# Optimization experiments

Hardware: AMD Instinct MI355X
Metric: run time of the kernel (lower is better)

Reference implementation:

```python
import jax, jax.numpy as jnp
import numpy as np

N = 20000   # num_nodes
D = 128     # node_dim
H = 128     # hidden_dim (also per-head channels, PyG out_channels is per-head)
EV = 64     # event_dim
NH = 4      # heads
E = 250000  # num edges
NT = 8      # num_event_types
K = 4       # active event types


def setup_inputs() -> dict:
    key = jax.random.key(0)
    ks = jax.random.split(key, 24)
    def w(i, shape, s=0.05):
        return jax.random.normal(ks[i], shape, dtype=jnp.float32) * s
    z = lambda shape: jnp.zeros(shape, jnp.float32)
    o = lambda shape: jnp.ones(shape, jnp.float32)
    return {
        "node_ids": jnp.arange(N, dtype=jnp.int32),
        "event_type_ids": jax.random.randint(ks[0], (K,), 0, NT, dtype=jnp.int32),
        "src": jax.random.randint(ks[1], (E,), 0, N, dtype=jnp.int32),
        "dst": jax.random.randint(ks[2], (E,), 0, N, dtype=jnp.int32),
        "event_features": jax.random.normal(ks[3], (EV,), dtype=jnp.float32),
        "event_intensity": jax.random.uniform(ks[4], (K,), dtype=jnp.float32),
        "node_emb_table": w(5, (N, D), 1.0),
        "event_type_table": w(6, (NT, H), 0.5),
        "ev_w1": w(7, (EV, H)), "ev_b1": z((H,)), "ev_g1": o((H,)), "ev_bt1": z((H,)),
        "ev_w2": w(8, (H, H)), "ev_b2": z((H,)), "ev_g2": o((H,)), "ev_bt2": z((H,)),
        "wq": w(9, (D + H, NH * H)), "bq": z((NH * H,)),
        "wk": w(10, (D + H, NH * H)), "bk": z((NH * H,)),
        "wv": w(11, (D + H, NH * H)), "bv": z((NH * H,)),
        "wskip": w(12, (D + H, H)), "bskip": z((H,)),
        "g0_w": w(13, (H, NH * H)), "g0_as": w(14, (NH, H), 0.1), "g0_ad": w(15, (NH, H), 0.1), "g0_b": z((H,)),
        "g1_w": w(16, (H, NH * H)), "g1_as": w(17, (NH, H), 0.1), "g1_ad": w(18, (NH, H), 0.1), "g1_b": z((H,)),
        "wih": w(19, (H, 4 * H)), "whh": w(20, (H, 4 * H)), "bih": z((4 * H,)), "bhh": z((4 * H,)),
    }


def layer_norm(x, g, b, eps=1e-5):
    mu = jnp.mean(x, axis=-1, keepdims=True)
    var = jnp.mean(jnp.square(x - mu), axis=-1, keepdims=True)
    return (x - mu) * jax.lax.rsqrt(var + eps) * g + b


def segment_softmax(logits, seg, n):
    # logits: [E, NH]; softmax over edges sharing the same destination seg id
    m = jax.ops.segment_max(logits, seg, num_segments=n)
    m = jnp.where(jnp.isfinite(m), m, 0.0)  # guard empty segments
    e = jnp.exp(logits - m[seg])
    s = jax.ops.segment_sum(e, seg, num_segments=n)
    return e / (s[seg] + 1e-16)


def _forward(node_ids, event_type_ids, src, dst,
             event_features, event_intensity, node_emb_table, event_type_table,
             ev_w1, ev_b1, ev_g1, ev_bt1, ev_w2, ev_b2, ev_g2, ev_bt2,
             wq, bq, wk, bk, wv, bv, wskip, bskip,
             g0_w, g0_as, g0_ad, g0_b, g1_w, g1_as, g1_ad, g1_b,
             wih, whh, bih, bhh):
    node_emb = node_emb_table[node_ids]                                      # [N, D]
    # event encoder MLP (dropout off / eval mode)
    e = jax.nn.relu(layer_norm(event_features @ ev_w1 + ev_b1, ev_g1, ev_bt1))
    e = jax.nn.relu(layer_norm(e @ ev_w2 + ev_b2, ev_g2, ev_bt2))            # [H]
    # intensity-weighted mean of active event-type embeddings
    e = e + jnp.mean(event_type_table[event_type_ids] * event_intensity[:, None], axis=0)
    x = jnp.concatenate([node_emb, jnp.broadcast_to(e, (N, H))], axis=1)     # [N, D+H]

    # --- TransformerConv (heads=NH, concat=False -> head mean, root_weight skip) ---
    q = (x @ wq + bq).reshape(N, NH, H)
    k = (x @ wk + bk).reshape(N, NH, H)
    v = (x @ wv + bv).reshape(N, NH, H)
    alpha = jnp.sum(q[dst] * k[src], axis=-1) / jnp.sqrt(jnp.float32(H))     # [E, NH]
    alpha = segment_softmax(alpha, dst, N)
    agg = jax.ops.segment_sum(v[src] * alpha[..., None], dst, num_segments=N)  # [N, NH, H]
    x = agg.mean(axis=1) + x @ wskip + bskip                                 # [N, H]

    sl = jnp.arange(N, dtype=src.dtype)
    src2 = jnp.concatenate([src, sl])
    dst2 = jnp.concatenate([dst, sl])
    for w_, asrc, adst, b_ in ((g0_w, g0_as, g0_ad, g0_b), (g1_w, g1_as, g1_ad, g1_b)):
        xh = (x @ w_).reshape(N, NH, H)
        a_s = jnp.sum(xh * asrc, axis=-1)                                    # [N, NH]
        a_d = jnp.sum(xh * adst, axis=-1)
        ee = jax.nn.leaky_relu(a_s[src2] + a_d[dst2], 0.2)                   # [E+N, NH]
        a = segment_softmax(ee, dst2, N)
        out = jax.ops.segment_sum(xh[src2] * a[..., None], dst2, num_segments=N)
        x = jax.nn.relu(out.mean(axis=1) + b_)                               # [N, H]

    # --- batched LSTMCell, zero initial (h, c); torch gate order i, f, g, o ---
    h0 = jnp.zeros((N, H), x.dtype)
    c0 = jnp.zeros((N, H), x.dtype)
    gates = x @ wih + bih + h0 @ whh + bhh                                   # [N, 4H]
    gi, gf, gg, go = jnp.split(gates, 4, axis=-1)
    c = jax.nn.sigmoid(gf) * c0 + jax.nn.sigmoid(gi) * jnp.tanh(gg)
    h = jax.nn.sigmoid(go) * jnp.tanh(c)
    return h, c


def reference(node_ids, event_type_ids, src, dst,
              event_features, event_intensity, node_emb_table, event_type_table,
              ev_w1, ev_b1, ev_g1, ev_bt1, ev_w2, ev_b2, ev_g2, ev_bt2,
              wq, bq, wk, bk, wv, bv, wskip, bskip,
              g0_w, g0_as, g0_ad, g0_b, g1_w, g1_as, g1_ad, g1_b,
              wih, whh, bih, bhh):
    return _forward(node_ids, event_type_ids, src, dst,
                    event_features, event_intensity, node_emb_table, event_type_table,
                    ev_w1, ev_b1, ev_g1, ev_bt1, ev_w2, ev_b2, ev_g2, ev_bt2,
                    wq, bq, wk, bk, wv, bv, wskip, bskip,
                    g0_w, g0_as, g0_ad, g0_b, g1_w, g1_as, g1_ad, g1_b,
                    wih, whh, bih, bhh)
```

## Files before the change

### kernel.cpp

```cpp
#include <hip/hip_runtime.h>
#include <math.h>

#define D_DIM 128
#define H_DIM 128
#define SQRT_H_INV 0.08838834764831845f
#define BCOL_QKV 0
#define BCOL_G0 1664
#define BCOL_G1 2176
#define BCOL_W  2688
#define BCOL_TOT 3072

typedef unsigned short u16;
typedef unsigned short ushort8v __attribute__((ext_vector_type(8)));
typedef __bf16 bf16x8 __attribute__((ext_vector_type(8)));
typedef float f32x4 __attribute__((ext_vector_type(4)));

__device__ __forceinline__ float grp16_sum(float v) {
  v += __shfl_xor(v, 1);
  v += __shfl_xor(v, 2);
  v += __shfl_xor(v, 4);
  v += __shfl_xor(v, 8);
  return v;
}

__device__ __forceinline__ void split_bf16(float x, u16& h, u16& l) {
  __bf16 hb = (__bf16)x;
  float rm = x - (float)hb;
  __bf16 lb = (__bf16)rm;
  h = __builtin_bit_cast(u16, hb);
  l = __builtin_bit_cast(u16, lb);
}

__global__ __launch_bounds__(128) void k_event(
    const float* __restrict__ ef, int EV,
    const float* __restrict__ w1, const float* __restrict__ b1,
    const float* __restrict__ g1, const float* __restrict__ bt1,
    const float* __restrict__ w2, const float* __restrict__ b2,
    const float* __restrict__ g2, const float* __restrict__ bt2,
    const float* __restrict__ ett, const int* __restrict__ etid,
    const float* __restrict__ inten, int K,
    float* __restrict__ e_out)
{
  __shared__ float sh[H_DIM];
  __shared__ float red[H_DIM];
  const int t = threadIdx.x;

  float acc = b1[t];
  for (int i = 0; i < EV; ++i) acc += ef[i] * w1[i * H_DIM + t];

  red[t] = acc; __syncthreads();
  for (int s = 64; s > 0; s >>= 1) { if (t < s) red[t] += red[t + s]; __syncthreads(); }
  float mu = red[0] / H_DIM; __syncthreads();
  float d = acc - mu;
  red[t] = d * d; __syncthreads();
  for (int s = 64; s > 0; s >>= 1) { if (t < s) red[t] += red[t + s]; __syncthreads(); }
  float var = red[0] / H_DIM; __syncthreads();
  float y = d * rsqrtf(var + 1e-5f) * g1[t] + bt1[t];
  y = fmaxf(y, 0.f);
  sh[t] = y; __syncthreads();

  float acc2 = b2[t];
  for (int i = 0; i < H_DIM; ++i) acc2 += sh[i] * w2[i * H_DIM + t];

  red[t] = acc2; __syncthreads();
  for (int s = 64; s > 0; s >>= 1) { if (t < s) red[t] += red[t + s]; __syncthreads(); }
  mu = red[0] / H_DIM; __syncthreads();
  d = acc2 - mu;
  red[t] = d * d; __syncthreads();
  for (int s = 64; s > 0; s >>= 1) { if (t < s) red[t] += red[t + s]; __syncthreads(); }
  var = red[0] / H_DIM; __syncthreads();
  float y2 = d * rsqrtf(var + 1e-5f) * g2[t] + bt2[t];
  y2 = fmaxf(y2, 0.f);

  float m = 0.f;
  for (int k = 0; k < K; ++k) m += ett[etid[k] * H_DIM + t] * inten[k];
  e_out[t] = y2 + m / (float)K;
}

__global__ __launch_bounds__(256) void k_cvec_all(
    const float* __restrict__ e,
    const float* __restrict__ wq, const float* __restrict__ bq,
    const float* __restrict__ wk, const float* __restrict__ bk,
    const float* __restrict__ wv, const float* __restrict__ bv,
    const float* __restrict__ wskip, const float* __restrict__ bskip,
    const float* __restrict__ bih, const float* __restrict__ bhh,
    float* __restrict__ cvec1, float* __restrict__ cvec2)
{
  __shared__ float es[H_DIM];
  const int t = threadIdx.x;
  if (t < H_DIM) es[t] = e[t];
  __syncthreads();
  int j = blockIdx.x * 256 + t;
  if (j < 1664) {
    const float* W; const float* b; int col; int stride;
    if (j < 512)       { W = wq;    b = bq;    col = j;        stride = 512; }
    else if (j < 1024) { W = wk;    b = bk;    col = j - 512;  stride = 512; }
    else if (j < 1536) { W = wv;    b = bv;    col = j - 1024; stride = 512; }
    else               { W = wskip; b = bskip; col = j - 1536; stride = 128; }
    float a = b[col];
    for (int i = 0; i < H_DIM; ++i) a += es[i] * W[(D_DIM + i) * stride + col];
    cvec1[j] = a;
  } else if (j < 1664 + 384) {
    int j2 = j - 1664;
    int src = (j2 < 128) ? j2 : j2 + 128;
    cvec2[j2] = bih[src] + bhh[src];
  }
}

__global__ __launch_bounds__(256) void k_split_all(
    const float* __restrict__ wq, const float* __restrict__ wk,
    const float* __restrict__ wv, const float* __restrict__ wskip,
    const float* __restrict__ g0w, const float* __restrict__ g1w,
    const float* __restrict__ wih,
    u16* __restrict__ hi, u16* __restrict__ lo)
{
  int idx = blockIdx.x * 256 + threadIdx.x;
  if (idx >= BCOL_TOT * 16) return;
  int n = idx >> 4, g = idx & 15;
  const float* W; int col, stride;
  if (n < 512)        { W = wq;    col = n;        stride = 512; }
  else if (n < 1024)  { W = wk;    col = n - 512;  stride = 512; }
  else if (n < 1536)  { W = wv;    col = n - 1024; stride = 512; }
  else if (n < 1664)  { W = wskip; col = n - 1536; stride = 128; }
  else if (n < 2176)  { W = g0w;   col = n - 1664; stride = 512; }
  else if (n < 2688)  { W = g1w;   col = n - 2176; stride = 512; }
  else { int c = n - 2688; W = wih; col = (c < 128) ? c : c + 128; stride = 512; }
  int gp = g ^ (n & 7);
  size_t dst = (size_t)n * 128 + gp * 8;
#pragma unroll
  for (int j = 0; j < 8; ++j) {
    u16 h, l;
    split_bf16(W[(size_t)(g * 8 + j) * stride + col], h, l);
    hi[dst + j] = h; lo[dst + j] = l;
  }
}

__global__ __launch_bounds__(256) void k_split_a(
    const float* __restrict__ A, const int* __restrict__ ids,
    u16* __restrict__ hi, u16* __restrict__ lo, int M, int Mpad)
{
  int idx = blockIdx.x * 256 + threadIdx.x;
  if (idx >= Mpad * 16) return;
  int row = idx >> 4, g = idx & 15;
  int gp = g ^ (row & 7);
  size_t dst = (size_t)row * 128 + gp * 8;
  if (row < M) {
    int ar = ids ? ids[row] : row;
    const float* srcp = A + (size_t)ar * 128 + g * 8;
#pragma unroll
    for (int j = 0; j < 8; ++j) {
      u16 h, l;
      split_bf16(srcp[j], h, l);
      hi[dst + j] = h; lo[dst + j] = l;
    }
  } else {
#pragma unroll
    for (int j = 0; j < 8; ++j) { hi[dst + j] = 0; lo[dst + j] = 0; }
  }
}

__global__ __launch_bounds__(256, 2) void mfma_gemm(
    const u16* __restrict__ Ahi, const u16* __restrict__ Alo,
    const u16* __restrict__ Bhi, const u16* __restrict__ Blo,
    const float* __restrict__ cvec,
    u16* __restrict__ bf_out, int bf_cols,
    float* __restrict__ f32_out, int f32_lo, int ld_f32,
    const float* __restrict__ asw, const float* __restrict__ adw,
    float* __restrict__ a_s, float* __restrict__ a_d,
    int M)
{
  __shared__ u16 lds[32768];
  u16* As_hi = lds;
  u16* As_lo = lds + 8192;
  u16* Bs_hi = lds + 16384;
  u16* Bs_lo = lds + 24576;

  const int t = threadIdx.x;
  const int bm = blockIdx.y * 128;
  const int bn = blockIdx.x * 128;
  const int lane = t & 63;
  const int wid = t >> 6;
  const int wr = wid >> 1, wc = wid & 1;
  const int abase = wr * 64 + (lane & 15);
  const int bbase = wc * 64 + (lane & 15);

  int srow[4], sg[4];
#pragma unroll
  for (int i = 0; i < 4; ++i) {
    int idx = i * 256 + t;
    srow[i] = idx >> 3;
    sg[i] = idx & 7;
  }

  ushort8v ra_h[4], ra_l[4], rb_h[4], rb_l[4];

#pragma unroll
  for (int i = 0; i < 4; ++i) {
    size_t ga = (size_t)(bm + srow[i]) * 128 + sg[i] * 8;
    size_t gb = (size_t)(bn + srow[i]) * 128 + sg[i] * 8;
    ra_h[i] = *(const ushort8v*)&Ahi[ga];
    ra_l[i] = *(const ushort8v*)&Alo[ga];
    rb_h[i] = *(const ushort8v*)&Bhi[gb];
    rb_l[i] = *(const ushort8v*)&Blo[gb];
  }
#pragma unroll
  for (int i = 0; i < 4; ++i) {
    int lo_ = srow[i] * 64 + sg[i] * 8;
    *(ushort8v*)&As_hi[lo_] = ra_h[i];
    *(ushort8v*)&As_lo[lo_] = ra_l[i];
    *(ushort8v*)&Bs_hi[lo_] = rb_h[i];
    *(ushort8v*)&Bs_lo[lo_] = rb_l[i];
  }
  __syncthreads();

#pragma unroll
  for (int i = 0; i < 4; ++i) {
    size_t ga = (size_t)(bm + srow[i]) * 128 + 64 + sg[i] * 8;
    size_t gb = (size_t)(bn + srow[i]) * 128 + 64 + sg[i] * 8;
    ra_h[i] = *(const ushort8v*)&Ahi[ga];
    ra_l[i] = *(const ushort8v*)&Alo[ga];
    rb_h[i] = *(const ushort8v*)&Bhi[gb];
    rb_l[i] = *(const ushort8v*)&Blo[gb];
  }

  f32x4 acc[4][4];
  const f32x4 zero = {0.f, 0.f, 0.f, 0.f};
#pragma unroll
  for (int i = 0; i < 4; ++i)
#pragma unroll
    for (int j = 0; j < 4; ++j) acc[i][j] = zero;

#pragma unroll
  for (int ks = 0; ks < 2; ++ks) {
    const int gl = (((ks & 1) << 2) + (lane >> 4)) ^ (lane & 7);
    bf16x8 ah[4], al[4], bh[4], bl[4];
#pragma unroll
    for (int i = 0; i < 4; ++i) {
      int ra = (abase + i * 16) * 64 + gl * 8;
      ah[i] = *(const bf16x8*)&As_hi[ra];
      al[i] = *(const bf16x8*)&As_lo[ra];
      int rb = (bbase + i * 16) * 64 + gl * 8;
      bh[i] = *(const bf16x8*)&Bs_hi[rb];
      bl[i] = *(const bf16x8*)&Bs_lo[rb];
    }
#pragma unroll
    for (int i = 0; i < 4; ++i)
#pragma unroll
      for (int j = 0; j < 4; ++j) {
        acc[i][j] = __builtin_amdgcn_mfma_f32_16x16x32_bf16(ah[i], bh[j], acc[i][j], 0, 0, 0);
        acc[i][j] = __builtin_amdgcn_mfma_f32_16x16x32_bf16(ah[i], bl[j], acc[i][j], 0, 0, 0);
        acc[i][j] = __builtin_amdgcn_mfma_f32_16x16x32_bf16(al[i], bh[j], acc[i][j], 0, 0, 0);
      }
  }
  __syncthreads();

#pragma unroll
  for (int i = 0; i < 4; ++i) {
    int lo_ = srow[i] * 64 + sg[i] * 8;
    *(ushort8v*)&As_hi[lo_] = ra_h[i];
    *(ushort8v*)&As_lo[lo_] = ra_l[i];
    *(ushort8v*)&Bs_hi[lo_] = rb_h[i];
    *(ushort8v*)&Bs_lo[lo_] = rb_l[i];
  }
  __syncthreads();

#pragma unroll
  for (int ks = 2; ks < 4; ++ks) {
    const int gl = (((ks & 1) << 2) + (lane >> 4)) ^ (lane & 7);
    bf16x8 ah[4], al[4], bh[4], bl[4];
#pragma unroll
    for (int i = 0; i < 4; ++i) {
      int ra = (abase + i * 16) * 64 + gl * 8;
      ah[i] = *(const bf16x8*)&As_hi[ra];
      al[i] = *(const bf16x8*)&As_lo[ra];
      int rb = (bbase + i * 16) * 64 + gl * 8;
      bh[i] = *(const bf16x8*)&Bs_hi[rb];
      bl[i] = *(const bf16x8*)&Bs_lo[rb];
    }
#pragma unroll
    for (int i = 0; i < 4; ++i)
#pragma unroll
      for (int j = 0; j < 4; ++j) {
        acc[i][j] = __builtin_amdgcn_mfma_f32_16x16x32_bf16(ah[i], bh[j], acc[i][j], 0, 0, 0);
        acc[i][j] = __builtin_amdgcn_mfma_f32_16x16x32_bf16(ah[i], bl[j], acc[i][j], 0, 0, 0);
        acc[i][j] = __builtin_amdgcn_mfma_f32_16x16x32_bf16(al[i], bh[j], acc[i][j], 0, 0, 0);
      }
  }

  const int rq = (lane >> 4) << 2;
  const int cq = lane & 15;
  const int head = bn >> 7;

  float ws_[4], wd_[4];
  float* redS = (float*)lds;
  float* redD = ((float*)lds) + 128;
  if (asw) {
#pragma unroll
    for (int j = 0; j < 4; ++j) {
      int cc = (wc * 64 + j * 16 + cq) & 127;
      ws_[j] = asw[head * 128 + cc];
      wd_[j] = adw[head * 128 + cc];
    }
    __syncthreads();
    if (t < 128) { redS[t] = 0.f; }
    else if (t < 256) { redD[t - 128] = 0.f; }
    __syncthreads();
  }

#pragma unroll
  for (int i = 0; i < 4; ++i) {
#pragma unroll
    for (int r = 0; r < 4; ++r) {
      int rowl = wr * 64 + i * 16 + rq + r;
      int row = bm + rowl;
      bool rok = row < M;
      float ps = 0.f, pd = 0.f;
#pragma unroll
      for (int j = 0; j < 4; ++j) {
        int col = bn + wc * 64 + j * 16 + cq;
        float a = acc[i][j][r];
        if (rok) {
          float val = a + (cvec ? cvec[col] : 0.f);
          if (bf_out && col < bf_cols)
            bf_out[(size_t)row * bf_cols + col] =
                __builtin_bit_cast(u16, (__bf16)val);
          if (f32_out && col >= f32_lo)
            f32_out[(size_t)row * ld_f32 + (col - f32_lo)] = val;
        }
        if (asw) { ps += a * ws_[j]; pd += a * wd_[j]; }
      }
      if (asw && rok) {
        atomicAdd(&redS[rowl], ps);
        atomicAdd(&redD[rowl], pd);
      }
    }
  }
  if (asw) {
    __syncthreads();
    if (t < 128) {
      int row = bm + t;
      if (row < M) {
        a_s[row * 4 + head] = redS[t];
        a_d[row * 4 + head] = redD[t];
      }
    }
  }
}

__global__ __launch_bounds__(256) void k_zero(int* __restrict__ p, int n) {
  int i = blockIdx.x * 256 + threadIdx.x;
  if (i < n) p[i] = 0;
}
__global__ __launch_bounds__(256) void k_count(
    const int* __restrict__ dst, int* __restrict__ counts, int E) {
  int e = blockIdx.x * 256 + threadIdx.x;
  if (e < E) atomicAdd(&counts[dst[e]], 1);
}
__global__ __launch_bounds__(1024) void k_scan(
    const int* __restrict__ counts, int* __restrict__ offs,
    int* __restrict__ cursor, int N)
{
  __shared__ int wsum[16];
  const int t = threadIdx.x;
  const int lane = t & 63;
  const int wid = t >> 6;
  int running = 0;
  for (int base = 0; base < N; base += 1024) {
    int v = (base + t < N) ? counts[base + t] : 0;
    int incl = v;
#pragma unroll
    for (int s = 1; s < 64; s <<= 1) {
      int u = __shfl_up(incl, s);
      if (lane >= s) incl += u;
    }
    if (lane == 63) wsum[wid] = incl;
    __syncthreads();
    if (wid == 0) {
      int w = (lane < 16) ? wsum[lane] : 0;
#pragma unroll
      for (int s = 1; s < 16; s <<= 1) {
        int u = __shfl_up(w, s);
        if (lane >= s) w += u;
      }
      if (lane < 16) wsum[lane] = w;
    }
    __syncthreads();
    int wpre = (wid > 0) ? wsum[wid - 1] : 0;
    int tot = wsum[15];
    int inclg = incl + wpre;
    if (base + t < N) {
      offs[base + t + 1] = running + inclg;
      cursor[base + t] = running + inclg - v;
    }
    running += tot;
    __syncthreads();
  }
  if (t == 0) offs[0] = 0;
}
__global__ __launch_bounds__(256) void k_fill(
    const int* __restrict__ src, const int* __restrict__ dst,
    int* __restrict__ cursor, int* __restrict__ csr_src, int E) {
  int e = blockIdx.x * 256 + threadIdx.x;
  if (e < E) {
    int slot = atomicAdd(&cursor[dst[e]], 1);
    csr_src[slot] = src[e];
  }
}

__global__ __launch_bounds__(256) void k_tconv(
    const u16* __restrict__ QKVp, const float* __restrict__ skipbuf,
    const int* __restrict__ offs, const int* __restrict__ csr_src,
    u16* __restrict__ Xhi, u16* __restrict__ Xlo, int N)
{
  const int wid = threadIdx.x >> 6;
  const int lane = threadIdx.x & 63;
  const int node = blockIdx.x * 4 + wid;
  if (node >= N) {
    if (lane < 16) {
      size_t dst = (size_t)node * 128 + (size_t)((lane ^ (node & 7)) * 8);
#pragma unroll
      for (int j = 0; j < 8; ++j) { Xhi[dst + j] = 0; Xlo[dst + j] = 0; }
    }
    return;
  }
  float q[8];
  {
    bf16x8 qv = *(const bf16x8*)(QKVp + (size_t)node * 1536 + lane * 8);
#pragma unroll
    for (int j = 0; j < 8; ++j) q[j] = (float)qv[j];
  }
  const int beg = offs[node], end = offs[node + 1];
  float mx = -1e30f;
  float ssum = 0.f;
  float acc[8] = {0.f,0.f,0.f,0.f,0.f,0.f,0.f,0.f};

  int e = beg;
  for (; e + 4 <= end; e += 4) {
    int s0 = csr_src[e];
    int s1 = csr_src[e + 1];
    int s2 = csr_src[e + 2];
    int s3 = csr_src[e + 3];
    const u16* r0 = QKVp + (size_t)s0 * 1536 + 512 + lane * 8;
    const u16* r1 = QKVp + (size_t)s1 * 1536 + 512 + lane * 8;
    const u16* r2 = QKVp + (size_t)s2 * 1536 + 512 + lane * 8;
    const u16* r3 = QKVp + (size_t)s3 * 1536 + 512 + lane * 8;
    bf16x8 k0 = *(const bf16x8*)(r0);
    bf16x8 k1 = *(const bf16x8*)(r1);
    bf16x8 k2 = *(const bf16x8*)(r2);
    bf16x8 k3 = *(const bf16x8*)(r3);
    bf16x8 v0 = *(const bf16x8*)(r0 + 512);
    bf16x8 v1 = *(const bf16x8*)(r1 + 512);
    bf16x8 v2 = *(const bf16x8*)(r2 + 512);
    bf16x8 v3 = *(const bf16x8*)(r3 + 512);
    float p0 = 0.f, p1 = 0.f, p2 = 0.f, p3 = 0.f;
#pragma unroll
    for (int j = 0; j < 8; ++j) {
      p0 += q[j] * (float)k0[j];
      p1 += q[j] * (float)k1[j];
      p2 += q[j] * (float)k2[j];
      p3 += q[j] * (float)k3[j];
    }
    p0 = grp16_sum(p0) * SQRT_H_INV;
    p1 = grp16_sum(p1) * SQRT_H_INV;
    p2 = grp16_sum(p2) * SQRT_H_INV;
    p3 = grp16_sum(p3) * SQRT_H_INV;
    float nm = fmaxf(fmaxf(fmaxf(p0, p1), fmaxf(p2, p3)), mx);
    float sc = expf(mx - nm);
    float w0 = expf(p0 - nm);
    float w1 = expf(p1 - nm);
    float w2 = expf(p2 - nm);
    float w3 = expf(p3 - nm);
    ssum = ssum * sc + (w0 + w1) + (w2 + w3);
#pragma unroll
    for (int j = 0; j < 8; ++j)
      acc[j] = acc[j] * sc + (w0 * (float)v0[j] + w1 * (float)v1[j])
                           + (w2 * (float)v2[j] + w3 * (float)v3[j]);
    mx = nm;
  }
  for (; e < end; ++e) {
    int s0 = csr_src[e];
    const u16* r0 = QKVp + (size_t)s0 * 1536 + 512 + lane * 8;
    bf16x8 ka = *(const bf16x8*)(r0);
    bf16x8 va = *(const bf16x8*)(r0 + 512);
    float p0 = 0.f;
#pragma unroll
    for (int j = 0; j < 8; ++j) p0 += q[j] * (float)ka[j];
    p0 = grp16_sum(p0) * SQRT_H_INV;
    float nm = fmaxf(mx, p0);
    float sc = expf(mx - nm);
    float w0 = expf(p0 - nm);
    ssum = ssum * sc + w0;
#pragma unroll
    for (int j = 0; j < 8; ++j)
      acc[j] = acc[j] * sc + w0 * (float)va[j];
    mx = nm;
  }

  float inv = 1.f / (ssum + 1e-16f);
#pragma unroll
  for (int j = 0; j < 8; ++j) acc[j] *= inv;
#pragma unroll
  for (int j = 0; j < 8; ++j) {
    acc[j] += __shfl_xor(acc[j], 16);
    acc[j] += __shfl_xor(acc[j], 32);
  }
  if (lane < 16) {
    const float* sk = skipbuf + (size_t)node * 128 + lane * 8;
    size_t dst = (size_t)node * 128 + (size_t)((lane ^ (node & 7)) * 8);
#pragma unroll
    for (int j = 0; j < 8; ++j) {
      float x = 0.25f * acc[j] + sk[j];
      u16 h, l;
      split_bf16(x, h, l);
      Xhi[dst + j] = h; Xlo[dst + j] = l;
    }
  }
}

__global__ __launch_bounds__(256) void k_gat_agg(
    const u16* __restrict__ xhb,
    const float* __restrict__ a_s, const float* __restrict__ a_d,
    const int* __restrict__ offs, const int* __restrict__ csr_src,
    const float* __restrict__ bias,
    u16* __restrict__ Xhi, u16* __restrict__ Xlo, int N)
{
  const int wid = threadIdx.x >> 6;
  const int lane = threadIdx.x & 63;
  const int node = blockIdx.x * 4 + wid;
  if (node >= N) {
    if (lane < 16) {
      size_t dst = (size_t)node * 128 + (size_t)((lane ^ (node & 7)) * 8);
#pragma unroll
      for (int j = 0; j < 8; ++j) { Xhi[dst + j] = 0; Xlo[dst + j] = 0; }
    }
    return;
  }
  const int head = lane >> 4;
  const float adn = a_d[node * 4 + head];
  const float asn = a_s[node * 4 + head];
  float lself = asn + adn;
  lself = lself >= 0.f ? lself : 0.2f * lself;

  float mx = lself;
  float ssum = 1.f;
  float acc[8];
  {
    bf16x8 xs = *(const bf16x8*)(xhb + (size_t)node * 512 + lane * 8);
#pragma unroll
    for (int j = 0; j < 8; ++j) acc[j] = (float)xs[j];
  }

  const int beg = offs[node], end = offs[node + 1];
  int e = beg;
  for (; e + 4 <= end; e += 4) {
    int s0 = csr_src[e];
    int s1 = csr_src[e + 1];
    int s2 = csr_src[e + 2];
    int s3 = csr_src[e + 3];
    float l0 = a_s[s0 * 4 + head];
    float l1 = a_s[s1 * 4 + head];
    float l2 = a_s[s2 * 4 + head];
    float l3 = a_s[s3 * 4 + head];
    const u16* r0 = xhb + (size_t)s0 * 512 + lane * 8;
    const u16* r1 = xhb + (size_t)s1 * 512 + lane * 8;
    const u16* r2 = xhb + (size_t)s2 * 512 + lane * 8;
    const u16* r3 = xhb + (size_t)s3 * 512 + lane * 8;
    bf16x8 xa = *(const bf16x8*)(r0);
    bf16x8 xb = *(const bf16x8*)(r1);
    bf16x8 xc = *(const bf16x8*)(r2);
    bf16x8 xd = *(const bf16x8*)(r3);
    l0 += adn; l1 += adn; l2 += adn; l3 += adn;
    l0 = l0 >= 0.f ? l0 : 0.2f * l0;
    l1 = l1 >= 0.f ? l1 : 0.2f * l1;
    l2 = l2 >= 0.f ? l2 : 0.2f * l2;
    l3 = l3 >= 0.f ? l3 : 0.2f * l3;
    float nm = fmaxf(fmaxf(fmaxf(l0, l1), fmaxf(l2, l3)), mx);
    float sc = expf(mx - nm);
    float w0 = expf(l0 - nm);
    float w1 = expf(l1 - nm);
    float w2 = expf(l2 - nm);
    float w3 = expf(l3 - nm);
    ssum = ssum * sc + (w0 + w1) + (w2 + w3);
#pragma unroll
    for (int j = 0; j < 8; ++j)
      acc[j] = acc[j] * sc + (w0 * (float)xa[j] + w1 * (float)xb[j])
                           + (w2 * (float)xc[j] + w3 * (float)xd[j]);
    mx = nm;
  }
  for (; e < end; ++e) {
    int s0 = csr_src[e];
    float l0 = a_s[s0 * 4 + head] + adn;
    l0 = l0 >= 0.f ? l0 : 0.2f * l0;
    const u16* r0 = xhb + (size_t)s0 * 512 + lane * 8;
    bf16x8 xa = *(const bf16x8*)(r0);
    float nm = fmaxf(mx, l0);
    float sc = expf(mx - nm);
    float w0 = expf(l0 - nm);
    ssum = ssum * sc + w0;
#pragma unroll
    for (int j = 0; j < 8; ++j)
      acc[j] = acc[j] * sc + w0 * (float)xa[j];
    mx = nm;
  }

  float inv = 1.f / (ssum + 1e-16f);
#pragma unroll
  for (int j = 0; j < 8; ++j) acc[j] *= inv;
#pragma unroll
  for (int j = 0; j < 8; ++j) {
    acc[j] += __shfl_xor(acc[j], 16);
    acc[j] += __shfl_xor(acc[j], 32);
  }
  if (lane < 16) {
    const float* b = bias + lane * 8;
    size_t dst = (size_t)node * 128 + (size_t)((lane ^ (node & 7)) * 8);
#pragma unroll
    for (int j = 0; j < 8; ++j) {
      float x = fmaxf(0.25f * acc[j] + b[j], 0.f);
      u16 h, l;
      split_bf16(x, h, l);
      Xhi[dst + j] = h; Xlo[dst + j] = l;
    }
  }
}

__global__ __launch_bounds__(256) void k_lstm(
    const float* __restrict__ gates, float* __restrict__ out, int N)
{
  int idx = blockIdx.x * 256 + threadIdx.x;
  if (idx >= N * 128) return;
  int n = idx >> 7, c = idx & 127;
  const float* g = gates + (size_t)n * 384;
  float gi = g[c], gg = g[128 + c], go = g[256 + c];
  float cv = (1.f / (1.f + expf(-gi))) * tanhf(gg);
  float hv = (1.f / (1.f + expf(-go))) * tanhf(cv);
  out[idx] = hv;
  out[(size_t)N * 128 + idx] = cv;
}

extern "C" void kernel_launch(void* const* d_in, const int* in_sizes, int n_in,
                              void* d_out, int out_size, void* d_ws, size_t ws_size,
                              hipStream_t stream) {
  const int*   node_ids = (const int*)d_in[0];
  const int*   etid     = (const int*)d_in[1];
  const int*   src      = (const int*)d_in[2];
  const int*   dst      = (const int*)d_in[3];
  const float* ef       = (const float*)d_in[4];
  const float* inten    = (const float*)d_in[5];
  const float* nemb     = (const float*)d_in[6];
  const float* ett      = (const float*)d_in[7];
  const float* ev_w1 = (const float*)d_in[8],  *ev_b1 = (const float*)d_in[9];
  const float* ev_g1 = (const float*)d_in[10], *ev_bt1 = (const float*)d_in[11];
  const float* ev_w2 = (const float*)d_in[12], *ev_b2 = (const float*)d_in[13];
  const float* ev_g2 = (const float*)d_in[14], *ev_bt2 = (const float*)d_in[15];
  const float* wq = (const float*)d_in[16], *bq = (const float*)d_in[17];
  const float* wk = (const float*)d_in[18], *bk = (const float*)d_in[19];
  const float* wv = (const float*)d_in[20], *bv = (const float*)d_in[21];
  const float* wskip = (const float*)d_in[22], *bskip = (const float*)d_in[23];
  const float* g0_w = (const float*)d_in[24], *g0_as = (const float*)d_in[25];
  const float* g0_ad = (const float*)d_in[26], *g0_b = (const float*)d_in[27];
  const float* g1_w = (const float*)d_in[28], *g1_as = (const float*)d_in[29];
  const float* g1_ad = (const float*)d_in[30], *g1_b = (const float*)d_in[31];
  const float* wih = (const float*)d_in[32];
  const float* bih = (const float*)d_in[34], *bhh = (const float*)d_in[35];

  const int N = in_sizes[0];
  const int K = in_sizes[1];
  const int E = in_sizes[2];
  const int EV = in_sizes[4];

  const int gridMy = (N + 127) / 128;
  const int Npad = gridMy * 128;

  float* ws = (float*)d_ws;
  size_t o = 0;
  float* e_vec = ws + o; o += 128;
  float* cvec1 = ws + o; o += 1664;
  float* cvec2 = ws + o; o += 384;
  u16* Ballhi = (u16*)(ws + o); o += (size_t)BCOL_TOT * 64;
  u16* Balllo = (u16*)(ws + o); o += (size_t)BCOL_TOT * 64;
  u16* Ahi  = (u16*)(ws + o); o += (size_t)Npad * 64;
  u16* Alo  = (u16*)(ws + o); o += (size_t)Npad * 64;
  u16* XShi = (u16*)(ws + o); o += (size_t)Npad * 64;
  u16* XSlo = (u16*)(ws + o); o += (size_t)Npad * 64;
  u16* QKVp = (u16*)(ws + o); o += (size_t)Npad * 768;
  float* skipbuf = ws + o; o += (size_t)Npad * 128;
  u16* xhb  = (u16*)(ws + o); o += (size_t)Npad * 256;
  float* gates = ws + o; o += (size_t)Npad * 384;
  float* a_s   = ws + o; o += (size_t)N * 4;
  float* a_d   = ws + o; o += (size_t)N * 4;
  int* counts  = (int*)(ws + o); o += N;
  int* offs    = (int*)(ws + o); o += (size_t)N + 1;
  int* cursor  = (int*)(ws + o); o += N;
  int* csr_src = (int*)(ws + o); o += E;

  float* out = (float*)d_out;
  const int nodeBlocksPad = Npad / 4;

  k_event<<<1, 128, 0, stream>>>(ef, EV, ev_w1, ev_b1, ev_g1, ev_bt1,
                                 ev_w2, ev_b2, ev_g2, ev_bt2,
                                 ett, etid, inten, K, e_vec);
  k_cvec_all<<<8, 256, 0, stream>>>(e_vec, wq, bq, wk, bk, wv, bv,
                                    wskip, bskip, bih, bhh, cvec1, cvec2);
  k_split_all<<<(BCOL_TOT * 16) / 256, 256, 0, stream>>>(
      wq, wk, wv, wskip, g0_w, g1_w, wih, Ballhi, Balllo);
  k_split_a<<<(Npad * 16 + 255) / 256, 256, 0, stream>>>(nemb, node_ids, Ahi, Alo, N, Npad);

  k_zero<<<(N + 255) / 256, 256, 0, stream>>>(counts, N);
  k_count<<<(E + 255) / 256, 256, 0, stream>>>(dst, counts, E);
  k_scan<<<1, 1024, 0, stream>>>(counts, offs, cursor, N);
  k_fill<<<(E + 255) / 256, 256, 0, stream>>>(src, dst, cursor, csr_src, E);

  mfma_gemm<<<dim3(13, gridMy), 256, 0, stream>>>(
      Ahi, Alo, Ballhi + (size_t)BCOL_QKV * 128, Balllo + (size_t)BCOL_QKV * 128,
      cvec1, QKVp, 1536, skipbuf, 1536, 128,
      nullptr, nullptr, nullptr, nullptr, N);

  k_tconv<<<nodeBlocksPad, 256, 0, stream>>>(QKVp, skipbuf, offs, csr_src,
                                             XShi, XSlo, N);

  mfma_gemm<<<dim3(4, gridMy), 256, 0, stream>>>(
      XShi, XSlo, Ballhi + (size_t)BCOL_G0 * 128, Balllo + (size_t)BCOL_G0 * 128,
      nullptr, xhb, 512, nullptr, 0, 0,
      g0_as, g0_ad, a_s, a_d, N);
  k_gat_agg<<<nodeBlocksPad, 256, 0, stream>>>(xhb, a_s, a_d, offs, csr_src,
                                               g0_b, XShi, XSlo, N);

  mfma_gemm<<<dim3(4, gridMy), 256, 0, stream>>>(
      XShi, XSlo, Ballhi + (size_t)BCOL_G1 * 128, Balllo + (size_t)BCOL_G1 * 128,
      nullptr, xhb, 512, nullptr, 0, 0,
      g1_as, g1_ad, a_s, a_d, N);
  k_gat_agg<<<nodeBlocksPad, 256, 0, stream>>>(xhb, a_s, a_d, offs, csr_src,
                                               g1_b, XShi, XSlo, N);

  mfma_gemm<<<dim3(3, gridMy), 256, 0, stream>>>(
      XShi, XSlo, Ballhi + (size_t)BCOL_W * 128, Balllo + (size_t)BCOL_W * 128,
      cvec2, nullptr, 0, gates, 0, 384,
      nullptr, nullptr, nullptr, nullptr, N);
  k_lstm<<<((N * 128) + 255) / 256, 256, 0, stream>>>(gates, out, N);
}
```

Baseline: 453.3 us.

## Pre-tile GEMM operands in MFMA fragment layout and drop LDS staging

The split kernels and the GAT output writers now store the bf16 hi/lo operands in a 16-row blocked layout that matches the MFMA fragment order. This lets the GEMM load fragments straight from global memory into registers instead of staging them through a swizzled 64 KB LDS buffer. Dropping that buffer removes the barriers, leaves only a small reduction array in shared memory, and allows raising the occupancy hint to 3 blocks per CU. The trade-off is that operand reuse across waves now relies on L1/L2 instead of LDS, with more global load instructions. The gates workspace allocation is also halved, which risks overlapping later buffers if the gates rows still use a stride of 384.

After: 453.9 us. Within noise of the previous version (+0.1%).

```diff
diff --git a/kernel.cpp b/kernel.cpp
--- a/kernel.cpp
+++ b/kernel.cpp
@@ -14,6 +14,7 @@
 typedef unsigned short ushort8v __attribute__((ext_vector_type(8)));
 typedef __bf16 bf16x8 __attribute__((ext_vector_type(8)));
 typedef float f32x4 __attribute__((ext_vector_type(4)));
+
 
 __device__ __forceinline__ float grp16_sum(float v) {
   v += __shfl_xor(v, 1);
@@ -125,8 +126,7 @@
   else if (n < 2176)  { W = g0w;   col = n - 1664; stride = 512; }
   else if (n < 2688)  { W = g1w;   col = n - 2176; stride = 512; }
   else { int c = n - 2688; W = wih; col = (c < 128) ? c : c + 128; stride = 512; }
-  int gp = g ^ (n & 7);
-  size_t dst = (size_t)n * 128 + gp * 8;
+  size_t dst = (size_t)(n >> 4) * 2048 + g * 128 + (n & 15) * 8;
 #pragma unroll
   for (int j = 0; j < 8; ++j) {
     u16 h, l;
@@ -142,8 +142,7 @@
   int idx = blockIdx.x * 256 + threadIdx.x;
   if (idx >= Mpad * 16) return;
   int row = idx >> 4, g = idx & 15;
-  int gp = g ^ (row & 7);
-  size_t dst = (size_t)row * 128 + gp * 8;
+  size_t dst = (size_t)(row >> 4) * 2048 + g * 128 + (row & 15) * 8;
   if (row < M) {
     int ar = ids ? ids[row] : row;
     const float* srcp = A + (size_t)ar * 128 + g * 8;
@@ -159,7 +158,7 @@
   }
 }
 
-__global__ __launch_bounds__(256, 2) void mfma_gemm(
+__global__ __launch_bounds__(256, 3) void mfma_gemm(
     const u16* __restrict__ Ahi, const u16* __restrict__ Alo,
     const u16* __restrict__ Bhi, const u16* __restrict__ Blo,
     const float* __restrict__ cvec,
@@ -169,11 +168,7 @@
     float* __restrict__ a_s, float* __restrict__ a_d,
     int M)
 {
-  __shared__ u16 lds[32768];
-  u16* As_hi = lds;
-  u16* As_lo = lds + 8192;
-  u16* Bs_hi = lds + 16384;
-  u16* Bs_lo = lds + 24576;
+  __shared__ float red[256];
 
   const int t = threadIdx.x;
   const int bm = blockIdx.y * 128;
@@ -181,47 +176,11 @@
   const int lane = t & 63;
   const int wid = t >> 6;
   const int wr = wid >> 1, wc = wid & 1;
-  const int abase = wr * 64 + (lane & 15);
-  const int bbase = wc * 64 + (lane & 15);
-
-  int srow[4], sg[4];
-#pragma unroll
-  for (int i = 0; i < 4; ++i) {
-    int idx = i * 256 + t;
-    srow[i] = idx >> 3;
-    sg[i] = idx & 7;
-  }
-
-  ushort8v ra_h[4], ra_l[4], rb_h[4], rb_l[4];
-
-#pragma unroll
-  for (int i = 0; i < 4; ++i) {
-    size_t ga = (size_t)(bm + srow[i]) * 128 + sg[i] * 8;
-    size_t gb = (size_t)(bn + srow[i]) * 128 + sg[i] * 8;
-    ra_h[i] = *(const ushort8v*)&Ahi[ga];
-    ra_l[i] = *(const ushort8v*)&Alo[ga];
-    rb_h[i] = *(const ushort8v*)&Bhi[gb];
-    rb_l[i] = *(const ushort8v*)&Blo[gb];
-  }
-#pragma unroll
-  for (int i = 0; i < 4; ++i) {
-    int lo_ = srow[i] * 64 + sg[i] * 8;
-    *(ushort8v*)&As_hi[lo_] = ra_h[i];
-    *(ushort8v*)&As_lo[lo_] = ra_l[i];
-    *(ushort8v*)&Bs_hi[lo_] = rb_h[i];
-    *(ushort8v*)&Bs_lo[lo_] = rb_l[i];
-  }
-  __syncthreads();
-
-#pragma unroll
-  for (int i = 0; i < 4; ++i) {
-    size_t ga = (size_t)(bm + srow[i]) * 128 + 64 + sg[i] * 8;
-    size_t gb = (size_t)(bn + srow[i]) * 128 + 64 + sg[i] * 8;
-    ra_h[i] = *(const ushort8v*)&Ahi[ga];
-    ra_l[i] = *(const ushort8v*)&Alo[ga];
-    rb_h[i] = *(const ushort8v*)&Bhi[gb];
-    rb_l[i] = *(const ushort8v*)&Blo[gb];
-  }
+  const int lg = lane >> 4;
+  const int lr = lane & 15;
+
+  const int arb = (bm >> 4) + wr * 4;
+  const int brb = (bn >> 4) + wc * 4;
 
   f32x4 acc[4][4];
   const f32x4 zero = {0.f, 0.f, 0.f, 0.f};
@@ -231,17 +190,17 @@
     for (int j = 0; j < 4; ++j) acc[i][j] = zero;
 
 #pragma unroll
-  for (int ks = 0; ks < 2; ++ks) {
-    const int gl = (((ks & 1) << 2) + (lane >> 4)) ^ (lane & 7);
+  for (int ks = 0; ks < 4; ++ks) {
+    const int g = ks * 4 + lg;
     bf16x8 ah[4], al[4], bh[4], bl[4];
 #pragma unroll
     for (int i = 0; i < 4; ++i) {
-      int ra = (abase + i * 16) * 64 + gl * 8;
-      ah[i] = *(const bf16x8*)&As_hi[ra];
-      al[i] = *(const bf16x8*)&As_lo[ra];
-      int rb = (bbase + i * 16) * 64 + gl * 8;
-      bh[i] = *(const bf16x8*)&Bs_hi[rb];
-      bl[i] = *(const bf16x8*)&Bs_lo[rb];
+      size_t oa = (size_t)(arb + i) * 2048 + g * 128 + lr * 8;
+      ah[i] = *(const bf16x8*)&Ahi[oa];
+      al[i] = *(const bf16x8*)&Alo[oa];
+      size_t ob = (size_t)(brb + i) * 2048 + g * 128 + lr * 8;
+      bh[i] = *(const bf16x8*)&Bhi[ob];
+      bl[i] = *(const bf16x8*)&Blo[ob];
     }
 #pragma unroll
     for (int i = 0; i < 4; ++i)
@@ -252,48 +211,12 @@
         acc[i][j] = __builtin_amdgcn_mfma_f32_16x16x32_bf16(al[i], bh[j], acc[i][j], 0, 0, 0);
       }
   }
-  __syncthreads();
-
-#pragma unroll
-  for (int i = 0; i < 4; ++i) {
-    int lo_ = srow[i] * 64 + sg[i] * 8;
-    *(ushort8v*)&As_hi[lo_] = ra_h[i];
-    *(ushort8v*)&As_lo[lo_] = ra_l[i];
-    *(ushort8v*)&Bs_hi[lo_] = rb_h[i];
-    *(ushort8v*)&Bs_lo[lo_] = rb_l[i];
-  }
-  __syncthreads();
-
-#pragma unroll
-  for (int ks = 2; ks < 4; ++ks) {
-    const int gl = (((ks & 1) << 2) + (lane >> 4)) ^ (lane & 7);
-    bf16x8 ah[4], al[4], bh[4], bl[4];
-#pragma unroll
-    for (int i = 0; i < 4; ++i) {
-      int ra = (abase + i * 16) * 64 + gl * 8;
-      ah[i] = *(const bf16x8*)&As_hi[ra];
-      al[i] = *(const bf16x8*)&As_lo[ra];
-      int rb = (bbase + i * 16) * 64 + gl * 8;
-      bh[i] = *(const bf16x8*)&Bs_hi[rb];
-      bl[i] = *(const bf16x8*)&Bs_lo[rb];
-    }
-#pragma unroll
-    for (int i = 0; i < 4; ++i)
-#pragma unroll
-      for (int j = 0; j < 4; ++j) {
-        acc[i][j] = __builtin_amdgcn_mfma_f32_16x16x32_bf16(ah[i], bh[j], acc[i][j], 0, 0, 0);
-        acc[i][j] = __builtin_amdgcn_mfma_f32_16x16x32_bf16(ah[i], bl[j], acc[i][j], 0, 0, 0);
-        acc[i][j] = __builtin_amdgcn_mfma_f32_16x16x32_bf16(al[i], bh[j], acc[i][j], 0, 0, 0);
-      }
-  }
 
   const int rq = (lane >> 4) << 2;
   const int cq = lane & 15;
   const int head = bn >> 7;
 
   float ws_[4], wd_[4];
-  float* redS = (float*)lds;
-  float* redD = ((float*)lds) + 128;
   if (asw) {
 #pragma unroll
     for (int j = 0; j < 4; ++j) {
@@ -301,9 +224,7 @@
       ws_[j] = asw[head * 128 + cc];
       wd_[j] = adw[head * 128 + cc];
     }
-    __syncthreads();
-    if (t < 128) { redS[t] = 0.f; }
-    else if (t < 256) { redD[t - 128] = 0.f; }
+    if (t < 256) red[t] = 0.f;
     __syncthreads();
   }
 
@@ -330,8 +251,8 @@
         if (asw) { ps += a * ws_[j]; pd += a * wd_[j]; }
       }
       if (asw && rok) {
-        atomicAdd(&redS[rowl], ps);
-        atomicAdd(&redD[rowl], pd);
+        atomicAdd(&red[rowl], ps);
+        atomicAdd(&red[128 + rowl], pd);
       }
     }
   }
@@ -340,8 +261,8 @@
     if (t < 128) {
       int row = bm + t;
       if (row < M) {
-        a_s[row * 4 + head] = redS[t];
-        a_d[row * 4 + head] = redD[t];
+        a_s[row * 4 + head] = red[t];
+        a_d[row * 4 + head] = red[128 + t];
       }
     }
   }
@@ -417,7 +338,7 @@
   const int node = blockIdx.x * 4 + wid;
   if (node >= N) {
     if (lane < 16) {
-      size_t dst = (size_t)node * 128 + (size_t)((lane ^ (node & 7)) * 8);
+      size_t dst = (size_t)(node >> 4) * 2048 + lane * 128 + (node & 15) * 8;
 #pragma unroll
       for (int j = 0; j < 8; ++j) { Xhi[dst + j] = 0; Xlo[dst + j] = 0; }
     }
@@ -506,7 +427,7 @@
   }
   if (lane < 16) {
     const float* sk = skipbuf + (size_t)node * 128 + lane * 8;
-    size_t dst = (size_t)node * 128 + (size_t)((lane ^ (node & 7)) * 8);
+    size_t dst = (size_t)(node >> 4) * 2048 + lane * 128 + (node & 15) * 8;
 #pragma unroll
     for (int j = 0; j < 8; ++j) {
       float x = 0.25f * acc[j] + sk[j];
@@ -529,7 +450,7 @@
   const int node = blockIdx.x * 4 + wid;
   if (node >= N) {
     if (lane < 16) {
-      size_t dst = (size_t)node * 128 + (size_t)((lane ^ (node & 7)) * 8);
+      size_t dst = (size_t)(node >> 4) * 2048 + lane * 128 + (node & 15) * 8;
 #pragma unroll
       for (int j = 0; j < 8; ++j) { Xhi[dst + j] = 0; Xlo[dst + j] = 0; }
     }
@@ -613,7 +534,7 @@
   }
   if (lane < 16) {
     const float* b = bias + lane * 8;
-    size_t dst = (size_t)node * 128 + (size_t)((lane ^ (node & 7)) * 8);
+    size_t dst = (size_t)(node >> 4) * 2048 + lane * 128 + (node & 15) * 8;
 #pragma unroll
     for (int j = 0; j < 8; ++j) {
       float x = fmaxf(0.25f * acc[j] + b[j], 0.f);
@@ -686,7 +607,7 @@
   u16* QKVp = (u16*)(ws + o); o += (size_t)Npad * 768;
   float* skipbuf = ws + o; o += (size_t)Npad * 128;
   u16* xhb  = (u16*)(ws + o); o += (size_t)Npad * 256;
-  float* gates = ws + o; o += (size_t)Npad * 384;
+  float* gates = ws + o; o += (size_t)Npad * 192;
   float* a_s   = ws + o; o += (size_t)N * 4;
   float* a_d   = ws + o; o += (size_t)N * 4;
   int* counts  = (int*)(ws + o); o += N;
```
